# Kernel optimization log

Hardware: AMD Instinct MI355X
Metric: run time of the kernel (lower is better)

Reference implementation:

```python
import jax, jax.numpy as jnp
import numpy as np

IN_SHAPE_DOWN = (8, 16, 8)   # prod = 1024
OUT_SHAPE_DOWN = (4, 4, 4)   # prod = 64
TT_RANK = 8


def tt_to_dense(cores, in_shape, out_shape):
    """Contract TT-matrix cores [r_{k-1}, i_k, j_k, r_k] into a dense (prod_in, prod_out) matrix."""
    res = cores[0]  # [1, i1, j1, r1]
    for c in cores[1:]:
        res = jnp.einsum('...a,aijb->...ijb', res, c)
    res = res[0, ..., 0]  # (i1, j1, i2, j2, ..., id, jd)
    d = len(in_shape)
    perm = [2 * k for k in range(d)] + [2 * k + 1 for k in range(d)]
    return res.transpose(perm).reshape(int(np.prod(in_shape)), int(np.prod(out_shape)))


def setup_inputs() -> dict:
    key = jax.random.key(0)
    ks = jax.random.split(key, 8)
    r = TT_RANK
    # down cores: in factors (8,16,8) -> out factors (4,4,4)
    d1 = 0.1 * jax.random.normal(ks[0], (1, 8, 4, r), dtype=jnp.float32)
    d2 = 0.1 * jax.random.normal(ks[1], (r, 16, 4, r), dtype=jnp.float32)
    d3 = 0.1 * jax.random.normal(ks[2], (r, 8, 4, 1), dtype=jnp.float32)
    # up cores: shape = [reversed(out_down), reversed(in_down)] = [(4,4,4),(8,16,8)]
    u1 = 0.1 * jax.random.normal(ks[3], (1, 4, 8, r), dtype=jnp.float32)
    u2 = 0.1 * jax.random.normal(ks[4], (r, 4, 16, r), dtype=jnp.float32)
    u3 = 0.1 * jax.random.normal(ks[5], (r, 4, 8, 1), dtype=jnp.float32)
    x = jax.random.normal(ks[6], (4, 4096, 1024), dtype=jnp.float32)
    bias_down = 0.001 * jnp.ones((64,), dtype=jnp.float32)
    bias_up = 0.001 * jnp.ones((1024,), dtype=jnp.float32)
    return {"x": x, "d1": d1, "d2": d2, "d3": d3,
            "u1": u1, "u2": u2, "u3": u3,
            "bias_down": bias_down, "bias_up": bias_up}


def reference(x, d1, d2, d3, u1, u2, u3, bias_down, bias_up):
    # Down-project TT matrix: 1024 -> 64
    Wd = tt_to_dense([d1, d2, d3], IN_SHAPE_DOWN, OUT_SHAPE_DOWN)
    # Up-project TT matrix: 64 -> 1024 (reversed factor shapes)
    Wu = tt_to_dense([u1, u2, u3], tuple(reversed(OUT_SHAPE_DOWN)), tuple(reversed(IN_SHAPE_DOWN)))
    z = jnp.einsum('bsd,dk->bsk', x, Wd) + bias_down
    z = jax.nn.relu(z)
    y = jnp.einsum('bsk,kd->bsd', z, Wu) + bias_up
    return y
```

## Files before the change

### kernel.cpp

```cpp
#include <hip/hip_runtime.h>

typedef float f32x2 __attribute__((ext_vector_type(2)));
typedef float f32x4 __attribute__((ext_vector_type(4)));
typedef short short8 __attribute__((ext_vector_type(8)));

static __device__ __forceinline__ unsigned short f2bf(float f) {
    __bf16 h = (__bf16)f;
    return __builtin_bit_cast(unsigned short, h);
}

static __device__ __forceinline__ void gload_lds16(const void* g, void* l) {
    __builtin_amdgcn_global_load_lds(
        (const __attribute__((address_space(1))) void*)g,
        (__attribute__((address_space(3))) void*)l, 16, 0, 0);
}

__global__ __launch_bounds__(256) void tt_build_w_kernel(
    const float* __restrict__ d1, const float* __restrict__ d2, const float* __restrict__ d3,
    const float* __restrict__ u1, const float* __restrict__ u2, const float* __restrict__ u3,
    unsigned short* __restrict__ WdT_sw, unsigned short* __restrict__ WuT_sw)
{
    int t = blockIdx.x * 256 + threadIdx.x;
    if (t < 65536) {
        int j = t >> 10, i = t & 1023;
        int i1 = i >> 7, i2 = (i >> 3) & 15, i3 = i & 7;
        int j1 = j >> 4, j2 = (j >> 2) & 3, j3 = j & 3;
        float t3[8];
#pragma unroll
        for (int b = 0; b < 8; ++b) t3[b] = d3[(b * 8 + i3) * 4 + j3];
        float wsum = 0.f;
#pragma unroll
        for (int a = 0; a < 8; ++a) {
            float va = d1[(i1 * 4 + j1) * 8 + a];
            const float* p2 = d2 + ((a * 16 + i2) * 4 + j2) * 8;
            float wa = 0.f;
#pragma unroll
            for (int b = 0; b < 8; ++b) wa = fmaf(p2[b], t3[b], wa);
            wsum = fmaf(va, wa, wsum);
        }
        int w_ = i >> 8, ck = (i >> 6) & 3, ks2 = (i >> 5) & 1;
        int kg_ = (i >> 3) & 3, m = i & 7;
        int off = (w_ * 4 + ck) * 4096 + ((ks2 * 4 + kg_) * 64 + j) * 8 + m;
        WdT_sw[off] = f2bf(wsum);
    } else {
        int t2 = t - 65536;
        int d = t2 >> 6, k = t2 & 63;
        int k1 = k >> 4, k2 = (k >> 2) & 3, k3 = k & 3;
        int o1 = d >> 7, o2 = (d >> 3) & 15, o3 = d & 7;
        float t3[8];
#pragma unroll
        for (int b = 0; b < 8; ++b) t3[b] = u3[(b * 4 + k3) * 8 + o3];
        float wsum = 0.f;
#pragma unroll
        for (int a = 0; a < 8; ++a) {
            float va = u1[(k1 * 8 + o1) * 8 + a];
            const float* p2 = u2 + ((a * 4 + k2) * 16 + o2) * 8;
            float wa = 0.f;
#pragma unroll
            for (int b = 0; b < 8; ++b) wa = fmaf(p2[b], t3[b], wa);
            wsum = fmaf(va, wa, wsum);
        }
        int dl = d & 511, hf = d >> 9;
        int off = hf * 32768 + (dl * 8 + ((k >> 3) ^ (dl & 7))) * 8 + (k & 7);
        WuT_sw[off] = f2bf(wsum);
    }
}

__global__ __launch_bounds__(256) void tt_gemm1_kernel(
    const float* __restrict__ x, const unsigned short* __restrict__ WdT_sw,
    const float* __restrict__ bd, unsigned short* __restrict__ zbuf)
{
    __shared__ unsigned short wlds[4][2][4096];
    __shared__ float red[4][1024];
    const int t = threadIdx.x;
    const int lane = t & 63;
    const int w = t >> 6;
    const int l15 = lane & 15;
    const int kg = lane >> 4;
    const int tile0 = blockIdx.x * 2;

    const int colz = (t >> 6) * 16 + (t & 15);
    const int rowz = ((t & 63) >> 4) * 4;
    const float bdv = bd[colz];

    const unsigned short* wsrc = WdT_sw + w * 16384 + lane * 8;
    const float* xp0 = x + (size_t)(tile0 * 16 + l15) * 1024 + w * 256 + kg * 8;
    const float* xp1 = xp0 + 16 * 1024;

#pragma unroll
    for (int i = 0; i < 8; ++i)
        gload_lds16(wsrc + i * 512, &wlds[w][0][i * 512]);
#pragma unroll
    for (int i = 0; i < 8; ++i)
        gload_lds16(wsrc + 4096 + i * 512, &wlds[w][1][i * 512]);

    f32x4 xs[8];
    f32x4 acc0[4] = {{0.f, 0.f, 0.f, 0.f}, {0.f, 0.f, 0.f, 0.f},
                     {0.f, 0.f, 0.f, 0.f}, {0.f, 0.f, 0.f, 0.f}};
    f32x4 acc1[4] = {{0.f, 0.f, 0.f, 0.f}, {0.f, 0.f, 0.f, 0.f},
                     {0.f, 0.f, 0.f, 0.f}, {0.f, 0.f, 0.f, 0.f}};

#define XL8(o0, o1, o2, o3)                                                                        \
    asm volatile("global_load_dwordx4 %0, %1, off offset:" #o0 : "=v"(xs[0]) : "v"(xp0) : "memory"); \
    asm volatile("global_load_dwordx4 %0, %1, off offset:" #o1 : "=v"(xs[1]) : "v"(xp0) : "memory"); \
    asm volatile("global_load_dwordx4 %0, %1, off offset:" #o2 : "=v"(xs[2]) : "v"(xp0) : "memory"); \
    asm volatile("global_load_dwordx4 %0, %1, off offset:" #o3 : "=v"(xs[3]) : "v"(xp0) : "memory"); \
    asm volatile("global_load_dwordx4 %0, %1, off offset:" #o0 : "=v"(xs[4]) : "v"(xp1) : "memory"); \
    asm volatile("global_load_dwordx4 %0, %1, off offset:" #o1 : "=v"(xs[5]) : "v"(xp1) : "memory"); \
    asm volatile("global_load_dwordx4 %0, %1, off offset:" #o2 : "=v"(xs[6]) : "v"(xp1) : "memory"); \
    asm volatile("global_load_dwordx4 %0, %1, off offset:" #o3 : "=v"(xs[7]) : "v"(xp1) : "memory");

#define CPT(BUF) do {                                                                       \
    asm volatile("s_waitcnt vmcnt(0)" ::: "memory");                                        \
    __builtin_amdgcn_sched_barrier(0);                                                      \
    const unsigned short* lb = &wlds[w][BUF][0];                                            \
    _Pragma("unroll")                                                                       \
    for (int ks2 = 0; ks2 < 2; ++ks2) {                                                     \
        union { short8 v; unsigned short e[8]; } a0, a1;                                    \
        _Pragma("unroll")                                                                   \
        for (int e = 0; e < 4; ++e) {                                                       \
            a0.e[e] = f2bf(xs[ks2 * 2][e]);     a0.e[e + 4] = f2bf(xs[ks2 * 2 + 1][e]);     \
            a1.e[e] = f2bf(xs[4 + ks2 * 2][e]); a1.e[e + 4] = f2bf(xs[4 + ks2 * 2 + 1][e]); \
        }                                                                                   \
        _Pragma("unroll")                                                                   \
        for (int ct = 0; ct < 4; ++ct) {                                                    \
            short8 bf = *reinterpret_cast<const short8*>(                                   \
                lb + (ks2 * 4 + kg) * 512 + ct * 128 + l15 * 8);                            \
            acc0[ct] = __builtin_amdgcn_mfma_f32_16x16x32_bf16(a0.v, bf, acc0[ct], 0, 0, 0); \
            acc1[ct] = __builtin_amdgcn_mfma_f32_16x16x32_bf16(a1.v, bf, acc1[ct], 0, 0, 0); \
        }                                                                                   \
    }                                                                                       \
    __builtin_amdgcn_sched_barrier(0);                                                      \
} while (0)

    XL8(0, 16, 128, 144)
    CPT(0);
#pragma unroll
    for (int i = 0; i < 8; ++i)
        gload_lds16(wsrc + 2 * 4096 + i * 512, &wlds[w][0][i * 512]);
    XL8(256, 272, 384, 400)
    CPT(1);
#pragma unroll
    for (int i = 0; i < 8; ++i)
        gload_lds16(wsrc + 3 * 4096 + i * 512, &wlds[w][1][i * 512]);
    XL8(512, 528, 640, 656)
    CPT(0);
    XL8(768, 784, 896, 912)
    CPT(1);
#undef XL8
#undef CPT

#pragma unroll
    for (int ct = 0; ct < 4; ++ct)
        *reinterpret_cast<f32x4*>(&red[w][ct * 256 + lane * 4]) = acc0[ct];
    __syncthreads();
    {
        f32x4 v0 = *reinterpret_cast<const f32x4*>(&red[0][t * 4]);
        f32x4 v1 = *reinterpret_cast<const f32x4*>(&red[1][t * 4]);
        f32x4 v2 = *reinterpret_cast<const f32x4*>(&red[2][t * 4]);
        f32x4 v3 = *reinterpret_cast<const f32x4*>(&red[3][t * 4]);
#pragma unroll
        for (int r = 0; r < 4; ++r) {
            float zz = v0[r] + v1[r] + v2[r] + v3[r] + bdv;
            zz = zz > 0.f ? zz : 0.f;
            zbuf[tile0 * 1024 + (rowz + r) * 64 + colz] = f2bf(zz);
        }
    }
    __syncthreads();
#pragma unroll
    for (int ct = 0; ct < 4; ++ct)
        *reinterpret_cast<f32x4*>(&red[w][ct * 256 + lane * 4]) = acc1[ct];
    __syncthreads();
    {
        f32x4 v0 = *reinterpret_cast<const f32x4*>(&red[0][t * 4]);
        f32x4 v1 = *reinterpret_cast<const f32x4*>(&red[1][t * 4]);
        f32x4 v2 = *reinterpret_cast<const f32x4*>(&red[2][t * 4]);
        f32x4 v3 = *reinterpret_cast<const f32x4*>(&red[3][t * 4]);
#pragma unroll
        for (int r = 0; r < 4; ++r) {
            float zz = v0[r] + v1[r] + v2[r] + v3[r] + bdv;
            zz = zz > 0.f ? zz : 0.f;
            zbuf[(tile0 + 1) * 1024 + (rowz + r) * 64 + colz] = f2bf(zz);
        }
    }
}

__global__ __launch_bounds__(256) void tt_gemm2_kernel(
    const unsigned short* __restrict__ zbuf, const unsigned short* __restrict__ WuT_sw,
    const float* __restrict__ bu, float* __restrict__ y)
{
    __shared__ unsigned short wlds[32768];
    const int t = threadIdx.x;
    const int lane = t & 63;
    const int w = t >> 6;
    const int l15 = lane & 15;
    const int kg = lane >> 4;
    const int ch = blockIdx.x & 1;
    const int rg = blockIdx.x >> 1;

    const unsigned short* src = WuT_sw + ch * 32768 + w * 8192 + lane * 8;
#pragma unroll
    for (int i = 0; i < 16; ++i)
        gload_lds16(src + i * 512, &wlds[w * 8192 + i * 512]);

    f32x4 bv[8];
#pragma unroll
    for (int i = 0; i < 8; ++i)
        bv[i] = *reinterpret_cast<const f32x4*>(bu + ch * 512 + w * 128 + i * 16 + kg * 4);
    __syncthreads();

#pragma unroll
    for (int tt = 0; tt < 8; ++tt) {
        const int tile = rg * 8 + tt;
        short8 az0 = *reinterpret_cast<const short8*>(zbuf + tile * 1024 + l15 * 64 + kg * 8);
        short8 az1 = *reinterpret_cast<const short8*>(zbuf + tile * 1024 + l15 * 64 + 32 + kg * 8);
        const size_t yb = (size_t)(tile * 16 + l15) * 1024 + ch * 512 + w * 128;
#pragma unroll
        for (int i = 0; i < 8; ++i) {
            const int row = w * 128 + i * 16 + l15;
            const int s = row & 7;
            short8 b0 = *reinterpret_cast<const short8*>(&wlds[(row * 8 + (kg ^ s)) * 8]);
            short8 b1 = *reinterpret_cast<const short8*>(&wlds[(row * 8 + ((kg + 4) ^ s)) * 8]);
            f32x4 c = {0.f, 0.f, 0.f, 0.f};
            c = __builtin_amdgcn_mfma_f32_16x16x32_bf16(b0, az0, c, 0, 0, 0);
            c = __builtin_amdgcn_mfma_f32_16x16x32_bf16(b1, az1, c, 0, 0, 0);
            f32x4 o;
#pragma unroll
            for (int r = 0; r < 4; ++r) o[r] = c[r] + bv[i][r];
            *reinterpret_cast<f32x4*>(y + yb + i * 16 + kg * 4) = o;
        }
    }
}

extern "C" void kernel_launch(void* const* d_in, const int* in_sizes, int n_in,
                              void* d_out, int out_size, void* d_ws, size_t ws_size,
                              hipStream_t stream) {
    const float* x  = (const float*)d_in[0];
    const float* d1 = (const float*)d_in[1];
    const float* d2 = (const float*)d_in[2];
    const float* d3 = (const float*)d_in[3];
    const float* u1 = (const float*)d_in[4];
    const float* u2 = (const float*)d_in[5];
    const float* u3 = (const float*)d_in[6];
    const float* bd = (const float*)d_in[7];
    const float* bu = (const float*)d_in[8];
    float* y = (float*)d_out;
    unsigned short* WdT_sw = (unsigned short*)d_ws;
    unsigned short* WuT_sw = WdT_sw + 65536;
    unsigned short* zbuf   = WuT_sw + 65536;

    hipLaunchKernelGGL(tt_build_w_kernel, dim3(512), dim3(256), 0, stream,
                       d1, d2, d3, u1, u2, u3, WdT_sw, WuT_sw);
    hipLaunchKernelGGL(tt_gemm1_kernel, dim3(512), dim3(256), 0, stream,
                       x, WdT_sw, bd, zbuf);
    hipLaunchKernelGGL(tt_gemm2_kernel, dim3(256), dim3(256), 0, stream,
                       zbuf, WuT_sw, bu, y);
}
```

Baseline: 36.36 us.

## Restructure gemm1 into 512-thread blocks sharing the full down-weight in LDS

gemm1 now runs 256 blocks of 512 threads, each handling four row tiles, with two wave groups. Each group cooperatively loads half of the full 128 KB bf16 down-projection weight into dynamic LDS once, instead of each block streaming four weight chunks through double buffers. x loads are double-buffered in registers with partial vmcnt waits, and the cross-wave reduction is done in one pass with packed bf16x2 stores to zbuf. This trades 128 KB of LDS per block (one block per CU, fewer blocks) for less redundant weight traffic and fewer barriers.

```diff
diff --git a/kernel.cpp b/kernel.cpp
--- a/kernel.cpp
+++ b/kernel.cpp
@@ -38,9 +38,9 @@
             for (int b = 0; b < 8; ++b) wa = fmaf(p2[b], t3[b], wa);
             wsum = fmaf(va, wa, wsum);
         }
-        int w_ = i >> 8, ck = (i >> 6) & 3, ks2 = (i >> 5) & 1;
+        int q_ = i >> 8, ck = (i >> 6) & 3, ks2 = (i >> 5) & 1;
         int kg_ = (i >> 3) & 3, m = i & 7;
-        int off = (w_ * 4 + ck) * 4096 + ((ks2 * 4 + kg_) * 64 + j) * 8 + m;
+        int off = (q_ * 4 + ck) * 4096 + ((ks2 * 4 + kg_) * 64 + j) * 8 + m;
         WdT_sw[off] = f2bf(wsum);
     } else {
         int t2 = t - 65536;
@@ -66,66 +66,74 @@
     }
 }
 
-__global__ __launch_bounds__(256) void tt_gemm1_kernel(
+__global__ __launch_bounds__(512) void tt_gemm1_kernel(
     const float* __restrict__ x, const unsigned short* __restrict__ WdT_sw,
     const float* __restrict__ bd, unsigned short* __restrict__ zbuf)
 {
-    __shared__ unsigned short wlds[4][2][4096];
-    __shared__ float red[4][1024];
+    extern __shared__ unsigned short wlds[];
     const int t = threadIdx.x;
     const int lane = t & 63;
     const int w = t >> 6;
+    const int p = w >> 2;
+    const int h = w & 3;
     const int l15 = lane & 15;
     const int kg = lane >> 4;
-    const int tile0 = blockIdx.x * 2;
-
-    const int colz = (t >> 6) * 16 + (t & 15);
-    const int rowz = ((t & 63) >> 4) * 4;
-    const float bdv = bd[colz];
-
-    const unsigned short* wsrc = WdT_sw + w * 16384 + lane * 8;
-    const float* xp0 = x + (size_t)(tile0 * 16 + l15) * 1024 + w * 256 + kg * 8;
+    const int tile0 = blockIdx.x * 4;
+
+    const int uq = (t & 127) * 2;
+    const int tl = t >> 7;
+    const int colz = (uq >> 6) * 16 + (uq & 15);
+    const int rowz = ((uq & 63) >> 4) * 4;
+    const f32x2 bdv = *reinterpret_cast<const f32x2*>(bd + colz);
+
+    {
+        const unsigned short* src = WdT_sw + (h * 4 + 2 * p) * 4096 + lane * 8;
+        unsigned short* dst = wlds + h * 16384 + 2 * p * 4096;
+#pragma unroll
+        for (int i = 0; i < 16; ++i)
+            gload_lds16(src + i * 512, dst + i * 512);
+    }
+
+    const float* xp0 = x + ((size_t)(tile0 + 2 * p) * 16 + l15) * 1024 + h * 256 + kg * 8;
     const float* xp1 = xp0 + 16 * 1024;
-
-#pragma unroll
-    for (int i = 0; i < 8; ++i)
-        gload_lds16(wsrc + i * 512, &wlds[w][0][i * 512]);
-#pragma unroll
-    for (int i = 0; i < 8; ++i)
-        gload_lds16(wsrc + 4096 + i * 512, &wlds[w][1][i * 512]);
-
-    f32x4 xs[8];
+    const unsigned short* lb = wlds + h * 16384;
+
+    f32x4 xa[8], xb[8];
+#define XL8(D, o0, o1, o2, o3)                                                                     \
+    asm volatile("global_load_dwordx4 %0, %1, off offset:" #o0 : "=v"(D[0]) : "v"(xp0) : "memory"); \
+    asm volatile("global_load_dwordx4 %0, %1, off offset:" #o1 : "=v"(D[1]) : "v"(xp0) : "memory"); \
+    asm volatile("global_load_dwordx4 %0, %1, off offset:" #o2 : "=v"(D[2]) : "v"(xp0) : "memory"); \
+    asm volatile("global_load_dwordx4 %0, %1, off offset:" #o3 : "=v"(D[3]) : "v"(xp0) : "memory"); \
+    asm volatile("global_load_dwordx4 %0, %1, off offset:" #o0 : "=v"(D[4]) : "v"(xp1) : "memory"); \
+    asm volatile("global_load_dwordx4 %0, %1, off offset:" #o1 : "=v"(D[5]) : "v"(xp1) : "memory"); \
+    asm volatile("global_load_dwordx4 %0, %1, off offset:" #o2 : "=v"(D[6]) : "v"(xp1) : "memory"); \
+    asm volatile("global_load_dwordx4 %0, %1, off offset:" #o3 : "=v"(D[7]) : "v"(xp1) : "memory");
+
+    XL8(xa, 0, 16, 128, 144)
+    asm volatile("s_waitcnt vmcnt(8)" ::: "memory");
+    __syncthreads();
+
     f32x4 acc0[4] = {{0.f, 0.f, 0.f, 0.f}, {0.f, 0.f, 0.f, 0.f},
                      {0.f, 0.f, 0.f, 0.f}, {0.f, 0.f, 0.f, 0.f}};
     f32x4 acc1[4] = {{0.f, 0.f, 0.f, 0.f}, {0.f, 0.f, 0.f, 0.f},
                      {0.f, 0.f, 0.f, 0.f}, {0.f, 0.f, 0.f, 0.f}};
 
-#define XL8(o0, o1, o2, o3)                                                                        \
-    asm volatile("global_load_dwordx4 %0, %1, off offset:" #o0 : "=v"(xs[0]) : "v"(xp0) : "memory"); \
-    asm volatile("global_load_dwordx4 %0, %1, off offset:" #o1 : "=v"(xs[1]) : "v"(xp0) : "memory"); \
-    asm volatile("global_load_dwordx4 %0, %1, off offset:" #o2 : "=v"(xs[2]) : "v"(xp0) : "memory"); \
-    asm volatile("global_load_dwordx4 %0, %1, off offset:" #o3 : "=v"(xs[3]) : "v"(xp0) : "memory"); \
-    asm volatile("global_load_dwordx4 %0, %1, off offset:" #o0 : "=v"(xs[4]) : "v"(xp1) : "memory"); \
-    asm volatile("global_load_dwordx4 %0, %1, off offset:" #o1 : "=v"(xs[5]) : "v"(xp1) : "memory"); \
-    asm volatile("global_load_dwordx4 %0, %1, off offset:" #o2 : "=v"(xs[6]) : "v"(xp1) : "memory"); \
-    asm volatile("global_load_dwordx4 %0, %1, off offset:" #o3 : "=v"(xs[7]) : "v"(xp1) : "memory");
-
-#define CPT(BUF) do {                                                                       \
-    asm volatile("s_waitcnt vmcnt(0)" ::: "memory");                                        \
+#define CPT(XS, CKOFF, WN) do {                                                             \
+    asm volatile("s_waitcnt vmcnt(" #WN ")" ::: "memory");                                  \
     __builtin_amdgcn_sched_barrier(0);                                                      \
-    const unsigned short* lb = &wlds[w][BUF][0];                                            \
+    const unsigned short* lb_ = lb + CKOFF;                                                 \
     _Pragma("unroll")                                                                       \
     for (int ks2 = 0; ks2 < 2; ++ks2) {                                                     \
         union { short8 v; unsigned short e[8]; } a0, a1;                                    \
         _Pragma("unroll")                                                                   \
         for (int e = 0; e < 4; ++e) {                                                       \
-            a0.e[e] = f2bf(xs[ks2 * 2][e]);     a0.e[e + 4] = f2bf(xs[ks2 * 2 + 1][e]);     \
-            a1.e[e] = f2bf(xs[4 + ks2 * 2][e]); a1.e[e + 4] = f2bf(xs[4 + ks2 * 2 + 1][e]); \
+            a0.e[e] = f2bf(XS[ks2 * 2][e]);     a0.e[e + 4] = f2bf(XS[ks2 * 2 + 1][e]);     \
+            a1.e[e] = f2bf(XS[4 + ks2 * 2][e]); a1.e[e + 4] = f2bf(XS[4 + ks2 * 2 + 1][e]); \
         }                                                                                   \
         _Pragma("unroll")                                                                   \
         for (int ct = 0; ct < 4; ++ct) {                                                    \
             short8 bf = *reinterpret_cast<const short8*>(                                   \
-                lb + (ks2 * 4 + kg) * 512 + ct * 128 + l15 * 8);                            \
+                lb_ + (ks2 * 4 + kg) * 512 + ct * 128 + l15 * 8);                           \
             acc0[ct] = __builtin_amdgcn_mfma_f32_16x16x32_bf16(a0.v, bf, acc0[ct], 0, 0, 0); \
             acc1[ct] = __builtin_amdgcn_mfma_f32_16x16x32_bf16(a1.v, bf, acc1[ct], 0, 0, 0); \
         }                                                                                   \
@@ -133,54 +141,47 @@
     __builtin_amdgcn_sched_barrier(0);                                                      \
 } while (0)
 
-    XL8(0, 16, 128, 144)
-    CPT(0);
-#pragma unroll
-    for (int i = 0; i < 8; ++i)
-        gload_lds16(wsrc + 2 * 4096 + i * 512, &wlds[w][0][i * 512]);
-    XL8(256, 272, 384, 400)
-    CPT(1);
-#pragma unroll
-    for (int i = 0; i < 8; ++i)
-        gload_lds16(wsrc + 3 * 4096 + i * 512, &wlds[w][1][i * 512]);
-    XL8(512, 528, 640, 656)
-    CPT(0);
-    XL8(768, 784, 896, 912)
-    CPT(1);
+    XL8(xb, 256, 272, 384, 400)
+    CPT(xa, 0, 8);
+    XL8(xa, 512, 528, 640, 656)
+    CPT(xb, 4096, 8);
+    XL8(xb, 768, 784, 896, 912)
+    CPT(xa, 8192, 8);
+    CPT(xb, 12288, 0);
 #undef XL8
 #undef CPT
 
-#pragma unroll
-    for (int ct = 0; ct < 4; ++ct)
-        *reinterpret_cast<f32x4*>(&red[w][ct * 256 + lane * 4]) = acc0[ct];
-    __syncthreads();
+    __syncthreads();
+
+    float* red = reinterpret_cast<float*>(wlds);
     {
-        f32x4 v0 = *reinterpret_cast<const f32x4*>(&red[0][t * 4]);
-        f32x4 v1 = *reinterpret_cast<const f32x4*>(&red[1][t * 4]);
-        f32x4 v2 = *reinterpret_cast<const f32x4*>(&red[2][t * 4]);
-        f32x4 v3 = *reinterpret_cast<const f32x4*>(&red[3][t * 4]);
+        float* rp = red + p * 8192 + h * 2048;
+#pragma unroll
+        for (int ct = 0; ct < 4; ++ct) {
+            *reinterpret_cast<f32x4*>(rp + ct * 256 + lane * 4) = acc0[ct];
+            *reinterpret_cast<f32x4*>(rp + 1024 + ct * 256 + lane * 4) = acc1[ct];
+        }
+    }
+    __syncthreads();
+
+    {
+        const int pp = tl >> 1, tp = tl & 1;
+        const float* base = red + pp * 8192 + tp * 1024 + uq * 4;
+        f32x4 s0 = {0.f, 0.f, 0.f, 0.f}, s1 = {0.f, 0.f, 0.f, 0.f};
+#pragma unroll
+        for (int hh = 0; hh < 4; ++hh) {
+            f32x4 v0 = *reinterpret_cast<const f32x4*>(base + hh * 2048);
+            f32x4 v1 = *reinterpret_cast<const f32x4*>(base + hh * 2048 + 4);
+#pragma unroll
+            for (int r = 0; r < 4; ++r) { s0[r] += v0[r]; s1[r] += v1[r]; }
+        }
+        const int tile = tile0 + tl;
 #pragma unroll
         for (int r = 0; r < 4; ++r) {
-            float zz = v0[r] + v1[r] + v2[r] + v3[r] + bdv;
-            zz = zz > 0.f ? zz : 0.f;
-            zbuf[tile0 * 1024 + (rowz + r) * 64 + colz] = f2bf(zz);
-        }
-    }
-    __syncthreads();
-#pragma unroll
-    for (int ct = 0; ct < 4; ++ct)
-        *reinterpret_cast<f32x4*>(&red[w][ct * 256 + lane * 4]) = acc1[ct];
-    __syncthreads();
-    {
-        f32x4 v0 = *reinterpret_cast<const f32x4*>(&red[0][t * 4]);
-        f32x4 v1 = *reinterpret_cast<const f32x4*>(&red[1][t * 4]);
-        f32x4 v2 = *reinterpret_cast<const f32x4*>(&red[2][t * 4]);
-        f32x4 v3 = *reinterpret_cast<const f32x4*>(&red[3][t * 4]);
-#pragma unroll
-        for (int r = 0; r < 4; ++r) {
-            float zz = v0[r] + v1[r] + v2[r] + v3[r] + bdv;
-            zz = zz > 0.f ? zz : 0.f;
-            zbuf[(tile0 + 1) * 1024 + (rowz + r) * 64 + colz] = f2bf(zz);
+            float z0 = s0[r] + bdv[0]; z0 = z0 > 0.f ? z0 : 0.f;
+            float z1 = s1[r] + bdv[1]; z1 = z1 > 0.f ? z1 : 0.f;
+            unsigned int pk = (unsigned int)f2bf(z0) | ((unsigned int)f2bf(z1) << 16);
+            *reinterpret_cast<unsigned int*>(zbuf + tile * 1024 + (rowz + r) * 64 + colz) = pk;
         }
     }
 }
@@ -189,7 +190,7 @@
     const unsigned short* __restrict__ zbuf, const unsigned short* __restrict__ WuT_sw,
     const float* __restrict__ bu, float* __restrict__ y)
 {
-    __shared__ unsigned short wlds[32768];
+    __shared__ unsigned short wlds2[32768];
     const int t = threadIdx.x;
     const int lane = t & 63;
     const int w = t >> 6;
@@ -201,7 +202,7 @@
     const unsigned short* src = WuT_sw + ch * 32768 + w * 8192 + lane * 8;
 #pragma unroll
     for (int i = 0; i < 16; ++i)
-        gload_lds16(src + i * 512, &wlds[w * 8192 + i * 512]);
+        gload_lds16(src + i * 512, &wlds2[w * 8192 + i * 512]);
 
     f32x4 bv[8];
 #pragma unroll
@@ -219,8 +220,8 @@
         for (int i = 0; i < 8; ++i) {
             const int row = w * 128 + i * 16 + l15;
             const int s = row & 7;
-            short8 b0 = *reinterpret_cast<const short8*>(&wlds[(row * 8 + (kg ^ s)) * 8]);
-            short8 b1 = *reinterpret_cast<const short8*>(&wlds[(row * 8 + ((kg + 4) ^ s)) * 8]);
+            short8 b0 = *reinterpret_cast<const short8*>(&wlds2[(row * 8 + (kg ^ s)) * 8]);
+            short8 b1 = *reinterpret_cast<const short8*>(&wlds2[(row * 8 + ((kg + 4) ^ s)) * 8]);
             f32x4 c = {0.f, 0.f, 0.f, 0.f};
             c = __builtin_amdgcn_mfma_f32_16x16x32_bf16(b0, az0, c, 0, 0, 0);
             c = __builtin_amdgcn_mfma_f32_16x16x32_bf16(b1, az1, c, 0, 0, 0);
@@ -251,7 +252,7 @@
 
     hipLaunchKernelGGL(tt_build_w_kernel, dim3(512), dim3(256), 0, stream,
                        d1, d2, d3, u1, u2, u3, WdT_sw, WuT_sw);
-    hipLaunchKernelGGL(tt_gemm1_kernel, dim3(512), dim3(256), 0, stream,
+    hipLaunchKernelGGL(tt_gemm1_kernel, dim3(256), dim3(512), 131072, stream,
                        x, WdT_sw, bd, zbuf);
     hipLaunchKernelGGL(tt_gemm2_kernel, dim3(256), dim3(256), 0, stream,
                        zbuf, WuT_sw, bu, y);
```

New measurement: 37.75 us. 3.8% more time.
